# Performance work log

Measured on AMD Instinct MI355X. Metric: run time of the kernel, lower is better.

## Reference

```python
import jax, jax.numpy as jnp
import numpy as np

B_SZ = 4; SEQ = 2048; D_INPUT = 40; D_MODEL = 128; N_LAYERS = 4
D_STATE = 16; EXPAND = 2; D_INNER = D_MODEL * EXPAND
N_HEADS = 4; D_HEAD = D_MODEL // N_HEADS; MAX_LANDMARKS = 100
EPS_RMS = 1.1920929e-07  # torch nn.RMSNorm default eps = finfo(float32).eps
EPS_LN = 1e-5
A_FLOOR = 1e-4


def _rms(x, w):
    return x * jax.lax.rsqrt(jnp.mean(x * x, -1, keepdims=True) + EPS_RMS) * w


def _ln(x, w, b):
    m = jnp.mean(x, -1, keepdims=True)
    v = jnp.mean((x - m) ** 2, -1, keepdims=True)
    return (x - m) * jax.lax.rsqrt(v + EPS_LN) * w + b


def _mamba3_block(xin, Wi, Wx, Wdt, bdt, Alog, Bb, Cb, Bnw, Cnw, rf, Dv, Wo):
    # xin: (B,L,d_model)
    xz = xin @ Wi                       # (B,L,2*d_inner)
    xp, z = jnp.split(xz, 2, axis=-1)
    xp = jax.nn.silu(xp)
    sp = xp @ Wx                        # (B,L,2*d_state+2)
    B_raw = sp[..., :D_STATE]
    C_raw = sp[..., D_STATE:2 * D_STATE]
    dt_in = sp[..., -2:-1]
    lam_in = sp[..., -1:]
    Bm = _rms(B_raw + Bb, Bnw)
    Cm = _rms(C_raw + Cb, Cnw)
    dt = jax.nn.softplus(dt_in @ Wdt + bdt)   # (B,L,d_inner)
    lam = jax.nn.sigmoid(lam_in)              # (B,L,1)
    # data-dependent RoPE on B and C
    freqs = jax.nn.softplus(rf)                                  # (d_state//2,)
    ang = jnp.cumsum(jnp.mean(dt, -1, keepdims=True), axis=1) * freqs  # (B,L,ds/2)
    ca, sa = jnp.cos(ang), jnp.sin(ang)

    def rot(M):
        e, o = M[..., ::2], M[..., 1::2]
        return jnp.stack([e * ca - o * sa, e * sa + o * ca], -1).reshape(M.shape)

    Bm, Cm = rot(Bm), rot(Cm)
    A = jnp.minimum(-jnp.exp(Alog), -A_FLOOR)   # (d_inner,d_state)
    dte = dt[..., None]                          # (B,L,d_inner,1)
    dA = jnp.exp(A * dte)                        # (B,L,d_inner,d_state)
    Bx = Bm[:, :, None, :] * xp[..., None]       # (B,L,d_inner,d_state)
    Bx_prev = jnp.concatenate([jnp.zeros_like(Bx[:, :1]), Bx[:, :-1]], axis=1)
    lame = lam[..., None]                        # (B,L,1,1)
    u = (1.0 - lame) * dte * dA * Bx_prev + lame * dte * Bx
    u = u.at[:, 0].set(dte[:, 0] * Bx[:, 0])     # t==0 case: h = dt*B*x (no lambda)

    def step(h, inp):
        dA_t, u_t, C_t = inp
        h = dA_t * h + u_t
        return h, jnp.sum(h * C_t[:, None, :], -1)

    h0 = jnp.zeros((xin.shape[0], D_INNER, D_STATE), xin.dtype)
    _, ys = jax.lax.scan(step, h0, (jnp.swapaxes(dA, 0, 1), jnp.swapaxes(u, 0, 1), jnp.swapaxes(Cm, 0, 1)))
    y = jnp.swapaxes(ys, 0, 1)                   # (B,L,d_inner)
    y = y + xp * Dv
    y = y * jax.nn.silu(z)
    return y @ Wo


def _landmark_attn(mo, skip, hw, WQ, bQ, WK, bK, WV, bV, WO, bO):
    Bsz, L, Dm = skip.shape
    k = min(MAX_LANDMARKS, L)
    _, idx = jax.lax.top_k(hw, k)
    idx = jnp.sort(idx, axis=1)                            # (B,k)
    kv = jnp.take_along_axis(skip, idx[..., None], axis=1)  # (B,k,Dm)
    q = mo[:, -1:, :]                                       # (B,1,Dm)
    Q = (q @ WQ + bQ).reshape(Bsz, 1, N_HEADS, D_HEAD).transpose(0, 2, 1, 3)
    K = (kv @ WK + bK).reshape(Bsz, k, N_HEADS, D_HEAD).transpose(0, 2, 1, 3)
    V = (kv @ WV + bV).reshape(Bsz, k, N_HEADS, D_HEAD).transpose(0, 2, 1, 3)
    scores = jnp.einsum('bhqd,bhkd->bhqk', Q, K) * (D_HEAD ** -0.5)
    probs = jax.nn.softmax(scores, axis=-1)
    out = jnp.einsum('bhqk,bhkd->bhqd', probs, V).transpose(0, 2, 1, 3).reshape(Bsz, Dm)
    return out @ WO + bO


def setup_inputs() -> dict:
    key = jax.random.key(0)
    ks = iter(jax.random.split(key, 64))

    def nrm(shape, s=0.02):
        return jax.random.normal(next(ks), shape, jnp.float32) * s

    nl, ds, di, dm = N_LAYERS, D_STATE, D_INNER, D_MODEL
    inp = {}
    inp['x'] = jax.random.normal(next(ks), (B_SZ, SEQ, D_INPUT), jnp.float32)
    inp['hawkes_weights'] = jax.random.uniform(next(ks), (B_SZ, SEQ), jnp.float32)
    inp['emb_W'] = nrm((D_INPUT, dm)); inp['emb_b'] = jnp.zeros(dm, jnp.float32)
    inp['skip_W'] = nrm((D_INPUT, dm)); inp['skip_b'] = jnp.zeros(dm, jnp.float32)
    inp['in_proj_W'] = nrm((nl, dm, 2 * di))
    inp['x_proj_W'] = nrm((nl, di, 2 * ds + 2))
    inp['dt_proj_W'] = nrm((nl, 1, di), 1.0)
    inp['dt_proj_b'] = jnp.full((nl, di), -1.0, jnp.float32)
    inp['A_log'] = jnp.broadcast_to(jnp.log(jnp.arange(1, ds + 1, dtype=jnp.float32)), (nl, di, ds)) * jnp.ones((nl, di, ds), jnp.float32)
    inp['B_bias'] = jnp.ones((nl, ds), jnp.float32)
    inp['C_bias'] = jnp.ones((nl, ds), jnp.float32)
    inp['Bn_w'] = jnp.ones((nl, ds), jnp.float32)
    inp['Cn_w'] = jnp.ones((nl, ds), jnp.float32)
    inp['rope_freqs'] = nrm((nl, ds // 2), 0.01)
    inp['D_param'] = jnp.ones((nl, di), jnp.float32)
    inp['out_proj_W'] = nrm((nl, di, dm))
    inp['ln_w'] = jnp.ones((nl, dm), jnp.float32); inp['ln_b'] = jnp.zeros((nl, dm), jnp.float32)
    inp['fn_w'] = jnp.ones(dm, jnp.float32); inp['fn_b'] = jnp.zeros(dm, jnp.float32)
    for nm in ('Q', 'K', 'V', 'O'):
        inp['W' + nm] = nrm((dm, dm)); inp['b' + nm] = jnp.zeros(dm, jnp.float32)
    return inp


def reference(x, hawkes_weights, emb_W, emb_b, skip_W, skip_b, in_proj_W, x_proj_W,
              dt_proj_W, dt_proj_b, A_log, B_bias, C_bias, Bn_w, Cn_w, rope_freqs,
              D_param, out_proj_W, ln_w, ln_b, fn_w, fn_b, WQ, bQ, WK, bK, WV, bV, WO, bO):
    w = hawkes_weights[..., None]
    h = (x @ emb_W + emb_b) * w          # Hawkes-damped embedding for Mamba path
    skip = (x @ skip_W + skip_b) * w     # Hawkes skip for attention KV
    for i in range(N_LAYERS):
        h = h + _mamba3_block(_ln(h, ln_w[i], ln_b[i]), in_proj_W[i], x_proj_W[i],
                              dt_proj_W[i], dt_proj_b[i], A_log[i], B_bias[i], C_bias[i],
                              Bn_w[i], Cn_w[i], rope_freqs[i], D_param[i], out_proj_W[i])
    mo = _ln(h, fn_w, fn_b)
    return _landmark_attn(mo, skip, hawkes_weights, WQ, bQ, WK, bK, WV, bV, WO, bO)
```

## Files before the change

kernel.cpp:

```cpp
#include <hip/hip_runtime.h>
#include <hip/hip_fp16.h>
#include <math.h>

#define BSZ   4
#define SEQL  2048
#define DIN   40
#define DM    128
#define DI    256
#define DS    16
#define NL    4
#define NHEAD 4
#define DHEAD 32
#define KLM   100
#define NC    128
#define TC    16
#define NROWS 8
#define EROWS 16

typedef _Float16 v2h __attribute__((ext_vector_type(2)));

__device__ __forceinline__ float rcp_(float x){ return __builtin_amdgcn_rcpf(x); }
__device__ __forceinline__ float sigmoidf_(float x){ return rcp_(1.0f + __expf(-x)); }
__device__ __forceinline__ float siluf_(float x){ return x*rcp_(1.0f + __expf(-x)); }
__device__ __forceinline__ float softplusf_(float x){ return fmaxf(x,0.0f) + __logf(1.0f + __expf(-fabsf(x))); }
__device__ __forceinline__ float fdot2_(__half2 a, __half2 b, float c){
  return __builtin_amdgcn_fdot2(*(v2h*)&a, *(v2h*)&b, c, false);
}

__device__ __forceinline__ void load8(const float* p, float* r){
  const float4* q = (const float4*)p;
  float4 a=q[0], b=q[1];
  r[0]=a.x;r[1]=a.y;r[2]=a.z;r[3]=a.w; r[4]=b.x;r[5]=b.y;r[6]=b.z;r[7]=b.w;
}
__device__ __forceinline__ void store8(float* p, const float* r){
  float4* q = (float4*)p;
  q[0]=make_float4(r[0],r[1],r[2],r[3]);  q[1]=make_float4(r[4],r[5],r[6],r[7]);
}
__device__ __forceinline__ void load16(const float* p, float* r){
  load8(p, r); load8(p+8, r+8);
}
__device__ __forceinline__ void store16(float* p, const float* r){
  store8(p, r); store8(p+8, r+8);
}

__global__ __launch_bounds__(256) void prologue_kernel(
    const float* __restrict__ x, const float* __restrict__ hw,
    const float* __restrict__ eW, const float* __restrict__ eb,
    const float* __restrict__ sW, const float* __restrict__ sb,
    float* __restrict__ hb, float* __restrict__ sk,
    const float* __restrict__ inW, const float* __restrict__ outW,
    __half* __restrict__ Wip, __half* __restrict__ Wop,
    int* __restrict__ idxl_g)
{
  __shared__ float xr[EROWS][DIN];
  __shared__ int redcnt[2][4];
  __shared__ int eqc[8][4], gtc[8][4];

  const int blk = blockIdx.x;
  const int t = threadIdx.x;

  if (blk < 512){
    const size_t R0 = (size_t)blk * EROWS;
    for (int e=t; e<EROWS*DIN; e+=256) ((float*)xr)[e] = x[R0*DIN + e];
    __syncthreads();
    const int c = t & (DM-1), g = t >> 7;
    float ae[8], as[8];
    #pragma unroll
    for (int j=0;j<8;j++){ ae[j]=0.0f; as[j]=0.0f; }
    for (int k=0;k<DIN;k++){
      const float we  = eW[(size_t)k*DM + c];
      const float ws_ = sW[(size_t)k*DM + c];
      #pragma unroll
      for (int j=0;j<8;j++){
        const float xv = xr[g*8+j][k];
        ae[j] = fmaf(xv, we, ae[j]);
        as[j] = fmaf(xv, ws_, as[j]);
      }
    }
    const float ebv = eb[c], sbv = sb[c];
    #pragma unroll
    for (int j=0;j<8;j++){
      const size_t R = R0 + g*8 + j;
      const float w = hw[R];
      hb[R*DM + c] = (ae[j]+ebv)*w;
      sk[R*DM + c] = (as[j]+sbv)*w;
    }
  } else if (blk < 516){
    const int b = blk - 512;
    const int lane = t & 63, w = t >> 6;
    const float* hwp = hw + (size_t)b*SEQL;
    unsigned vb[8];
    #pragma unroll
    for (int q=0;q<8;q++) vb[q] = __float_as_uint(hwp[q*256 + t]);
    unsigned kth = 0u;
    for (int bit=31; bit>=0; --bit){
      const unsigned cand = kth | (1u << bit);
      int c0 = 0;
      #pragma unroll
      for (int q=0;q<8;q++) c0 += __popcll(__ballot(vb[q] >= cand));
      const int par = bit & 1;
      if (lane == 0) redcnt[par][w] = c0;
      __syncthreads();
      const int tot = redcnt[par][0]+redcnt[par][1]+redcnt[par][2]+redcnt[par][3];
      if (tot >= KLM) kth = cand;
    }
    unsigned long long beq[8], bgt[8];
    #pragma unroll
    for (int q=0;q<8;q++){
      beq[q] = __ballot(vb[q] == kth);
      bgt[q] = __ballot(vb[q] >  kth);
    }
    if (lane == 0){
      #pragma unroll
      for (int q=0;q<8;q++){ eqc[q][w] = __popcll(beq[q]); gtc[q][w] = __popcll(bgt[q]); }
    }
    __syncthreads();
    int gtTot = 0;
    #pragma unroll
    for (int q=0;q<8;q++) gtTot += gtc[q][0]+gtc[q][1]+gtc[q][2]+gtc[q][3];
    const int need_eq = KLM - gtTot;
    const unsigned long long lmask = (lane==0) ? 0ull : ((~0ull) >> (64-lane));
    int eqPfx = 0, gtPfx = 0;
    #pragma unroll
    for (int q=0;q<8;q++){
      int eqWP = 0, gtWP = 0;
      for (int w2=0; w2<w; ++w2){ eqWP += eqc[q][w2]; gtWP += gtc[q][w2]; }
      const int eqBefore = eqPfx + eqWP + __popcll(beq[q] & lmask);
      const int gtBefore = gtPfx + gtWP + __popcll(bgt[q] & lmask);
      if (vb[q] > kth){
        const int pos = gtBefore + min(eqBefore, need_eq);
        if (pos < KLM) idxl_g[b*KLM + pos] = q*256 + t;
      } else if (vb[q] == kth && eqBefore < need_eq){
        const int pos = gtBefore + eqBefore;
        if (pos < KLM) idxl_g[b*KLM + pos] = q*256 + t;
      }
      eqPfx += eqc[q][0]+eqc[q][1]+eqc[q][2]+eqc[q][3];
      gtPfx += gtc[q][0]+gtc[q][1]+gtc[q][2]+gtc[q][3];
    }
  } else {
    const int i = (blk - 516)*256 + t;
    if (i < NL*DM*2*DI){
      const int col = i & 511;
      const int klin = i >> 9;
      const int l = klin >> 7, k = klin & 127;
      Wip[(((size_t)(l*64 + (k>>1))*512 + col) << 1) + (k & 1)] = __float2half_rn(inW[i]);
    }
    if (i < NL*DI*DM){
      const int c = i & (DM-1);
      const int klin = i >> 7;
      const int l = klin >> 8, k = klin & 255;
      Wop[(((size_t)(l*128 + (k>>1))*DM + c) << 1) + (k & 1)] = __float2half_rn(outW[i]);
    }
  }
}

__global__ __launch_bounds__(256) void pre_kernel(
    const float* __restrict__ hb,
    const __half* __restrict__ Wip, const float* __restrict__ Wx,
    const float* __restrict__ Wdt, const float* __restrict__ bdt,
    const float* __restrict__ Bb, const float* __restrict__ Cb,
    const float* __restrict__ Bnw, const float* __restrict__ Cnw,
    const float* __restrict__ lnw, const float* __restrict__ lnb,
    __half* __restrict__ xph, __half* __restrict__ zsh,
    float* __restrict__ dtin, float* __restrict__ Shalf,
    float* __restrict__ Bmb, float* __restrict__ Cmb,
    float* __restrict__ lamb, float* __restrict__ mdtb)
{
  __shared__ __half2 xinh[NROWS][64+2];
  __shared__ float xps[NROWS][DI+4];
  __shared__ float spl[NROWS][40];
  __shared__ float pr[NROWS][4];

  const int t = threadIdx.x;
  const size_t R0 = (size_t)blockIdx.x * NROWS;

  {
    const int r = t >> 5, j = t & 31;
    const float4 v = ((const float4*)(hb + (R0 + r)*DM))[j];
    float s = v.x+v.y+v.z+v.w;
    #pragma unroll
    for (int o=16;o>0;o>>=1) s += __shfl_xor(s,o,32);
    const float m = s*(1.0f/DM);
    const float dx=v.x-m, dy=v.y-m, dz=v.z-m, dw=v.w-m;
    float ss = dx*dx+dy*dy+dz*dz+dw*dw;
    #pragma unroll
    for (int o=16;o>0;o>>=1) ss += __shfl_xor(ss,o,32);
    const float inv = 1.0f/sqrtf(ss*(1.0f/DM) + 1e-5f);
    const int c = j*4;
    const float v0 = dx*inv*lnw[c+0] + lnb[c+0];
    const float v1 = dy*inv*lnw[c+1] + lnb[c+1];
    const float v2 = dz*inv*lnw[c+2] + lnb[c+2];
    const float v3 = dw*inv*lnw[c+3] + lnb[c+3];
    xinh[r][2*j]   = __halves2half2(__float2half_rn(v0), __float2half_rn(v1));
    xinh[r][2*j+1] = __halves2half2(__float2half_rn(v2), __float2half_rn(v3));
  }
  __syncthreads();

  {
    float2 a[NROWS];
    #pragma unroll
    for (int r=0;r<NROWS;r++){ a[r].x=0.0f; a[r].y=0.0f; }
    const __half2* Wc = (const __half2*)Wip + 2*t;
    #pragma unroll 4
    for (int p=0;p<64;p++){
      const float2 wv = *(const float2*)&Wc[(size_t)p*512];
      const __half2 w0 = *(const __half2*)&wv.x;
      const __half2 w1 = *(const __half2*)&wv.y;
      #pragma unroll
      for (int r=0;r<NROWS;r++){
        const __half2 xv = xinh[r][p];
        a[r].x = fdot2_(xv, w0, a[r].x);
        a[r].y = fdot2_(xv, w1, a[r].y);
      }
    }
    if (t < 128){
      #pragma unroll
      for (int r=0;r<NROWS;r++){
        const float sx = siluf_(a[r].x), sy = siluf_(a[r].y);
        xps[r][2*t] = sx; xps[r][2*t+1] = sy;
        *(__half2*)&xph[(R0+r)*DI + 2*t] =
            __halves2half2(__float2half_rn(sx), __float2half_rn(sy));
      }
    } else {
      const int zc = 2*t - 2*DI + DI;
      #pragma unroll
      for (int r=0;r<NROWS;r++){
        const float sx = siluf_(a[r].x), sy = siluf_(a[r].y);
        *(__half2*)&zsh[(R0+r)*DI + zc] =
            __halves2half2(__float2half_rn(sx), __float2half_rn(sy));
      }
    }
  }
  __syncthreads();

  if (t < 136){
    const int r = t & 7, op = t >> 3;
    float ax=0.0f, ay=0.0f;
    for (int k=0;k<DI;k+=4){
      const float4 xv = *(const float4*)&xps[r][k];
      const float2 w0 = *(const float2*)&Wx[(size_t)(k+0)*34 + 2*op];
      const float2 w1 = *(const float2*)&Wx[(size_t)(k+1)*34 + 2*op];
      const float2 w2 = *(const float2*)&Wx[(size_t)(k+2)*34 + 2*op];
      const float2 w3 = *(const float2*)&Wx[(size_t)(k+3)*34 + 2*op];
      ax = fmaf(xv.x,w0.x,ax); ay = fmaf(xv.x,w0.y,ay);
      ax = fmaf(xv.y,w1.x,ax); ay = fmaf(xv.y,w1.y,ay);
      ax = fmaf(xv.z,w2.x,ax); ay = fmaf(xv.z,w2.y,ay);
      ax = fmaf(xv.w,w3.x,ax); ay = fmaf(xv.w,w3.y,ay);
    }
    spl[r][2*op] = ax; spl[r][2*op+1] = ay;
  }
  __syncthreads();

  {
    const int half = t >> 7;
    const int r2 = (t >> 4) & 7, s2 = t & 15;
    const float* bias = half ? Cb : Bb;
    const float* wn   = half ? Cnw : Bnw;
    const float v = spl[r2][half*DS + s2] + bias[s2];
    float ss = v*v;
    #pragma unroll
    for (int o=8;o>0;o>>=1) ss += __shfl_xor(ss,o,16);
    const float inv = 1.0f/sqrtf(ss*(1.0f/DS) + 1.1920929e-07f);
    (half ? Cmb : Bmb)[(R0+r2)*DS + s2] = v*inv*wn[s2];
  }

  {
    const int lane = t & 63, w = t >> 6;
    const float wdt = Wdt[t], bdtv = bdt[t];
    float Sd = 0.0f;
    #pragma unroll
    for (int r=0;r<NROWS;r++){
      const float dval = softplusf_(fmaf(spl[r][32], wdt, bdtv));
      Sd += dval;
      float s = dval;
      #pragma unroll
      for (int o=32;o>0;o>>=1) s += __shfl_xor(s,o,64);
      if (lane==0) pr[r][w] = s;
    }
    Shalf[(size_t)blockIdx.x * DI + t] = Sd;
    if (t < NROWS){
      lamb[R0+t] = sigmoidf_(spl[t][33]);
      dtin[R0+t] = spl[t][32];
    }
  }
  __syncthreads();
  if (t < NROWS)
    mdtb[R0+t] = (pr[t][0]+pr[t][1]+pr[t][2]+pr[t][3])*(1.0f/DI);
}

__global__ __launch_bounds__(512) void scan1_kernel(
    const __half* __restrict__ xph, const float* __restrict__ dtin,
    const float* __restrict__ Wdt, const float* __restrict__ bdt,
    const float* __restrict__ Bmb, const float* __restrict__ lamb,
    const float* __restrict__ mdtb, const float* __restrict__ rf,
    const float* __restrict__ Alog, float* __restrict__ hend)
{
  __shared__ float Bst[TC+1][DS];
  __shared__ float lst[TC];
  __shared__ float dsl[TC];
  __shared__ double fqs[8];
  __shared__ double wred[8];
  __shared__ double mloc[16];
  __shared__ __half xpl[TC+1][DI+8];
  const int t = threadIdx.x;
  const int d  = t >> 1;
  const int s0 = (t & 1) * 8;
  const int c = blockIdx.x & (NC-1);
  const int b = blockIdx.x >> 7;
  const size_t bL = (size_t)b*SEQL;
  const int t0 = c*TC;
  const int id = blockIdx.x*256 + d;

  if (t < 8){
    const double xfr = (double)rf[t];
    fqs[t] = fmax(xfr, 0.0) + log1p(exp(-fabs(xfr)));
  }
  {
    double s = 0.0;
    const int i0 = t*4;
    #pragma unroll
    for (int q=0;q<4;q++){
      const int idx = i0+q;
      s += (idx < t0) ? (double)mdtb[bL + idx] : 0.0;
    }
    #pragma unroll
    for (int o=32;o>0;o>>=1) s += __shfl_down(s,o,64);
    if ((t&63)==0) wred[t>>6] = s;
  }
  if (t >= 64 && t < 80) mloc[t-64] = (double)mdtb[bL + t0 + (t-64)];
  for (int e=t; e<(TC+1)*DS; e+=512){
    const int j = e >> 4, s = e & 15;
    const int trow = t0 - 1 + j;
    Bst[j][s] = (trow >= 0) ? Bmb[(bL + trow)*DS + s] : 0.0f;
  }
  for (int e=t; e<(TC+1)*DI; e+=512){
    const int j = e >> 8, dd = e & (DI-1);
    const int trow = t0 - 1 + j;
    xpl[j][dd] = (trow >= 0) ? xph[(bL + trow)*DI + dd] : __float2half_rn(0.0f);
  }
  if (t < TC){
    lst[t] = lamb[bL + t0 + t];
    dsl[t] = dtin[bL + t0 + t];
  }
  __syncthreads();
  if (t < 136){
    const int j = t >> 3, f = t & 7;
    const int trow = t0 - 1 + j;
    if (trow >= 0){
      double cs = wred[0]+wred[1]+wred[2]+wred[3]+wred[4]+wred[5]+wred[6]+wred[7];
      for (int i=0;i<j;i++) cs += mloc[i];
      const double ang = cs * fqs[f];
      const double red = ang - floor(ang*0.15915494309189535)*6.283185307179586;
      float sa, ca;
      __sincosf((float)red, &sa, &ca);
      const float e0 = Bst[j][2*f], o0 = Bst[j][2*f+1];
      Bst[j][2*f]   = e0*ca - o0*sa;
      Bst[j][2*f+1] = e0*sa + o0*ca;
    }
  }
  __syncthreads();

  float A[8];
  #pragma unroll
  for (int s=0;s<8;s++) A[s] = fminf(-__expf(Alog[d*DS + s0 + s]), -1e-4f);
  const float wdt = Wdt[d], bdtv = bdt[d];
  float h[8], Bprev[8];
  #pragma unroll
  for (int s=0;s<8;s++) h[s]=0.0f;
  float xpm1;
  int tstart;
  if (t0 > 0){
    #pragma unroll
    for (int s=0;s<8;s++) Bprev[s] = Bst[0][s0+s];
    xpm1 = __half2float(xpl[0][d]);
    tstart = 0;
  } else {
    const float dtv = softplusf_(fmaf(dsl[0], wdt, bdtv));
    const float xpv = __half2float(xpl[1][d]);
    #pragma unroll
    for (int s=0;s<8;s++){
      h[s] = dtv*(Bst[1][s0+s]*xpv);
      Bprev[s] = Bst[1][s0+s];
    }
    xpm1 = xpv;
    tstart = 1;
  }
  for (int j=tstart; j<TC; ++j){
    const float dtv = softplusf_(fmaf(dsl[j], wdt, bdtv));
    const float xpv = __half2float(xpl[j+1][d]);
    const float lamv = lst[j];
    const float dl = dtv*lamv;
    const float dml = dtv - dl;
    #pragma unroll
    for (int s=0;s<8;s++){
      const float a = __expf(A[s]*dtv);
      const float Bc = Bst[j+1][s0+s];
      const float u = fmaf(dml*a, Bprev[s]*xpm1, dl*(Bc*xpv));
      h[s] = fmaf(a, h[s], u);
      Bprev[s] = Bc;
    }
    xpm1 = xpv;
  }
  store8(hend + (size_t)id*DS + s0, h);
}

__global__ __launch_bounds__(128) void scan2_kernel(
    float* __restrict__ hend, const float* __restrict__ Shalf,
    const float* __restrict__ Alog)
{
  __shared__ float hS[NC][DS+1];
  __shared__ float pS[NC][DS+1];
  const int c = threadIdx.x;
  const int d = blockIdx.x & (DI-1);
  const int b = blockIdx.x >> 8;
  const float S = Shalf[(size_t)(b*(SEQL/NROWS) + 2*c)*DI + d]
                + Shalf[(size_t)(b*(SEQL/NROWS) + 2*c + 1)*DI + d];
  float P[DS], h[DS];
  #pragma unroll
  for (int s=0;s<DS;s++){
    const float A = fminf(-__expf(Alog[d*DS+s]), -1e-4f);
    P[s] = __expf(A*S);
  }
  load16(hend + (((size_t)(b*NC + c))*DI + d)*DS, h);
  #pragma unroll
  for (int s=0;s<DS;s++){ hS[c][s]=h[s]; pS[c][s]=P[s]; }
  __syncthreads();
  for (int off=1; off<NC; off<<=1){
    float hn[DS], pn[DS];
    const int src = c - off;
    if (src >= 0){
      #pragma unroll
      for (int s=0;s<DS;s++){ hn[s]=hS[src][s]; pn[s]=pS[src][s]; }
    }
    __syncthreads();
    if (src >= 0){
      #pragma unroll
      for (int s=0;s<DS;s++){
        h[s] = fmaf(P[s], hn[s], h[s]);
        P[s] *= pn[s];
        hS[c][s] = h[s]; pS[c][s] = P[s];
      }
    }
    __syncthreads();
  }
  float o[DS];
  if (c == 0){
    #pragma unroll
    for (int s=0;s<DS;s++) o[s] = 0.0f;
  } else {
    #pragma unroll
    for (int s=0;s<DS;s++) o[s] = hS[c-1][s];
  }
  store16(hend + (((size_t)(b*NC + c))*DI + d)*DS, o);
}

__global__ __launch_bounds__(512) void scan3post_kernel(
    const __half* __restrict__ xph, const float* __restrict__ dtin,
    const float* __restrict__ Wdt, const float* __restrict__ bdt,
    const float* __restrict__ Bmb, const float* __restrict__ Cmb,
    const float* __restrict__ lamb, const __half* __restrict__ zsh,
    const float* __restrict__ mdtb, const float* __restrict__ rf,
    const float* __restrict__ Alog, const float* __restrict__ Dv,
    const float* __restrict__ Hin, const __half* __restrict__ Wop,
    float* __restrict__ hb)
{
  __shared__ float Bst[TC+1][DS];
  __shared__ float Cst[TC][DS];
  __shared__ float lst[TC];
  __shared__ float dsl[TC];
  __shared__ double fqs[8];
  __shared__ double wred[8];
  __shared__ double mloc[16];
  __shared__ __half xpl[TC+1][DI+8];
  __shared__ __half zsl[TC][DI+8];
  __shared__ __half ysh[TC][DI+8];
  __shared__ float red[TC][132];
  const int t = threadIdx.x;
  const int d  = t >> 1;
  const int sh = t & 1;
  const int s0 = sh * 8;
  const int c = blockIdx.x & (NC-1);
  const int b = blockIdx.x >> 7;
  const size_t bL = (size_t)b*SEQL;
  const int t0 = c*TC;
  const int id = blockIdx.x*256 + d;

  if (t < 8){
    const double xfr = (double)rf[t];
    fqs[t] = fmax(xfr, 0.0) + log1p(exp(-fabs(xfr)));
  }
  {
    double s = 0.0;
    const int i0 = t*4;
    #pragma unroll
    for (int q=0;q<4;q++){
      const int idx = i0+q;
      s += (idx < t0) ? (double)mdtb[bL + idx] : 0.0;
    }
    #pragma unroll
    for (int o=32;o>0;o>>=1) s += __shfl_down(s,o,64);
    if ((t&63)==0) wred[t>>6] = s;
  }
  if (t >= 64 && t < 80) mloc[t-64] = (double)mdtb[bL + t0 + (t-64)];
  for (int e=t; e<(TC+1)*DS; e+=512){
    const int j = e >> 4, s = e & 15;
    const int trow = t0 - 1 + j;
    Bst[j][s] = (trow >= 0) ? Bmb[(bL + trow)*DS + s] : 0.0f;
    if (j < TC) Cst[j][s] = Cmb[(bL + t0 + j)*DS + s];
  }
  for (int e=t; e<(TC+1)*DI; e+=512){
    const int j = e >> 8, dd = e & (DI-1);
    const int trow = t0 - 1 + j;
    xpl[j][dd] = (trow >= 0) ? xph[(bL + trow)*DI + dd] : __float2half_rn(0.0f);
    if (j < TC) zsl[j][dd] = zsh[(bL + t0 + j)*DI + dd];
  }
  if (t < TC){
    lst[t] = lamb[bL + t0 + t];
    dsl[t] = dtin[bL + t0 + t];
  }
  __syncthreads();
  if (t < 264){
    const double base = wred[0]+wred[1]+wred[2]+wred[3]+wred[4]+wred[5]+wred[6]+wred[7];
    if (t < 136){
      const int j = t >> 3, f = t & 7;
      const int trow = t0 - 1 + j;
      if (trow >= 0){
        double cs = base;
        for (int i=0;i<j;i++) cs += mloc[i];
        const double ang = cs * fqs[f];
        const double rd = ang - floor(ang*0.15915494309189535)*6.283185307179586;
        float sa, ca;
        __sincosf((float)rd, &sa, &ca);
        const float e0 = Bst[j][2*f], o0 = Bst[j][2*f+1];
        Bst[j][2*f]   = e0*ca - o0*sa;
        Bst[j][2*f+1] = e0*sa + o0*ca;
      }
    } else {
      const int e2 = t - 136;
      const int j = e2 >> 3, f = e2 & 7;
      double cs = base;
      for (int i=0;i<=j;i++) cs += mloc[i];
      const double ang = cs * fqs[f];
      const double rd = ang - floor(ang*0.15915494309189535)*6.283185307179586;
      float sa, ca;
      __sincosf((float)rd, &sa, &ca);
      const float e0 = Cst[j][2*f], o0 = Cst[j][2*f+1];
      Cst[j][2*f]   = e0*ca - o0*sa;
      Cst[j][2*f+1] = e0*sa + o0*ca;
    }
  }
  __syncthreads();

  float A[8];
  #pragma unroll
  for (int s=0;s<8;s++) A[s] = fminf(-__expf(Alog[d*DS + s0 + s]), -1e-4f);
  const float wdt = Wdt[d], bdtv = bdt[d];
  const float dvp = Dv[d];
  float h[8], Bprev[8];
  load8(Hin + (size_t)id*DS + s0, h);
  float xpm1;
  int tstart;
  if (t0 > 0){
    #pragma unroll
    for (int s=0;s<8;s++) Bprev[s] = Bst[0][s0+s];
    xpm1 = __half2float(xpl[0][d]);
    tstart = 0;
  } else {
    const float dtv = softplusf_(fmaf(dsl[0], wdt, bdtv));
    const float xpv = __half2float(xpl[1][d]);
    float y = 0.0f;
    #pragma unroll
    for (int s=0;s<8;s++){
      h[s] = dtv*(Bst[1][s0+s]*xpv);
      y = fmaf(h[s], Cst[0][s0+s], y);
      Bprev[s] = Bst[1][s0+s];
    }
    const float ytot = y + __shfl_xor(y, 1, 64);
    if (sh == 0) ysh[0][d] = __float2half_rn((ytot + xpv*dvp)*__half2float(zsl[0][d]));
    xpm1 = xpv;
    tstart = 1;
  }
  for (int j=tstart; j<TC; ++j){
    const float dtv = softplusf_(fmaf(dsl[j], wdt, bdtv));
    const float xpv = __half2float(xpl[j+1][d]);
    const float lamv = lst[j];
    const float dl = dtv*lamv;
    const float dml = dtv - dl;
    float y = 0.0f;
    #pragma unroll
    for (int s=0;s<8;s++){
      const float a = __expf(A[s]*dtv);
      const float Bc = Bst[j+1][s0+s];
      const float u = fmaf(dml*a, Bprev[s]*xpm1, dl*(Bc*xpv));
      h[s] = fmaf(a, h[s], u);
      y = fmaf(h[s], Cst[j][s0+s], y);
      Bprev[s] = Bc;
    }
    const float ytot = y + __shfl_xor(y, 1, 64);
    if (sh == 0) ysh[j][d] = __float2half_rn((ytot + xpv*dvp)*__half2float(zsl[j][d]));
    xpm1 = xpv;
  }
  __syncthreads();

  {
    const int cg2  = t & 31;
    const int ks2  = (t >> 5) & 1;
    const int rg   = (t >> 6) & 3;
    const int ksHi = t >> 8;
    const int seg = ksHi*2 + ks2;
    const int k0p = seg*32;
    const int c0c = cg2*4;
    const __half2* Wp = (const __half2*)Wop;
    float acc[4][4];
    #pragma unroll
    for (int rr=0;rr<4;rr++){ acc[rr][0]=0.f; acc[rr][1]=0.f; acc[rr][2]=0.f; acc[rr][3]=0.f; }
    for (int kp=k0p; kp<k0p+32; ++kp){
      const float2 wv0 = *(const float2*)&Wp[(size_t)kp*DM + c0c];
      const float2 wv1 = *(const float2*)&Wp[(size_t)kp*DM + c0c + 2];
      const __half2 wc0 = *(const __half2*)&wv0.x;
      const __half2 wc1 = *(const __half2*)&wv0.y;
      const __half2 wc2 = *(const __half2*)&wv1.x;
      const __half2 wc3 = *(const __half2*)&wv1.y;
      #pragma unroll
      for (int rr=0;rr<4;rr++){
        const __half2 yv = *(const __half2*)&ysh[rg*4+rr][2*kp];
        acc[rr][0] = fdot2_(yv, wc0, acc[rr][0]);
        acc[rr][1] = fdot2_(yv, wc1, acc[rr][1]);
        acc[rr][2] = fdot2_(yv, wc2, acc[rr][2]);
        acc[rr][3] = fdot2_(yv, wc3, acc[rr][3]);
      }
    }
    #pragma unroll
    for (int rr=0;rr<4;rr++){
      #pragma unroll
      for (int cc=0;cc<4;cc++) acc[rr][cc] += __shfl_down(acc[rr][cc], 32, 64);
    }
    __syncthreads();
    const int lane = t & 63;
    if (ksHi == 1 && lane < 32){
      #pragma unroll
      for (int rr=0;rr<4;rr++)
        *(float4*)&red[rg*4+rr][c0c] = make_float4(acc[rr][0],acc[rr][1],acc[rr][2],acc[rr][3]);
    }
    __syncthreads();
    if (ksHi == 0 && lane < 32){
      #pragma unroll
      for (int rr=0;rr<4;rr++){
        const float4 rv = *(const float4*)&red[rg*4+rr][c0c];
        const size_t row = bL + t0 + rg*4 + rr;
        float4 hv = *(const float4*)&hb[row*DM + c0c];
        hv.x += acc[rr][0] + rv.x; hv.y += acc[rr][1] + rv.y;
        hv.z += acc[rr][2] + rv.z; hv.w += acc[rr][3] + rv.w;
        *(float4*)&hb[row*DM + c0c] = hv;
      }
    }
  }
}

__global__ __launch_bounds__(256) void attn_kernel(
    const float* __restrict__ hb, const float* __restrict__ sk,
    const int* __restrict__ idxl_g,
    const float* __restrict__ fnw, const float* __restrict__ fnb,
    const float* __restrict__ WQ, const float* __restrict__ bQ,
    const float* __restrict__ WK, const float* __restrict__ bK,
    const float* __restrict__ WV, const float* __restrict__ bV,
    const float* __restrict__ WO, const float* __restrict__ bO,
    float* __restrict__ outp)
{
  __shared__ float kv[KLM][DM+4];
  __shared__ float mo[DM];
  __shared__ float Qs[DM];
  __shared__ float qk[NHEAD][DM];
  __shared__ float bterm[NHEAD];
  __shared__ float sc[NHEAD][KLM];
  __shared__ float pbar[NHEAD][DM];
  __shared__ float attno[DM];
  const int b = blockIdx.x;
  const int t = threadIdx.x;
  const int lane = t & 63, w = t >> 6;

  if (t < 64){
    const float* hr = hb + ((size_t)b*SEQL + (SEQL-1))*DM;
    const float v0 = hr[t], v1 = hr[t+64];
    float s = v0+v1;
    #pragma unroll
    for (int o=32;o>0;o>>=1) s += __shfl_xor(s,o,64);
    const float m = s*(1.0f/DM);
    const float d0=v0-m, d1=v1-m;
    float ss = d0*d0 + d1*d1;
    #pragma unroll
    for (int o=32;o>0;o>>=1) ss += __shfl_xor(ss,o,64);
    const float inv = 1.0f/sqrtf(ss*(1.0f/DM) + 1e-5f);
    mo[t]    = d0*inv*fnw[t]    + fnb[t];
    mo[t+64] = d1*inv*fnw[t+64] + fnb[t+64];
  }
  for (int e=t; e<KLM*DM; e+=256){
    const int j = e >> 7, cc = e & (DM-1);
    kv[j][cc] = sk[((size_t)b*SEQL + idxl_g[b*KLM + j])*DM + cc];
  }
  __syncthreads();

  if (t < DM){
    float a = bQ[t];
    #pragma unroll 4
    for (int k=0;k<DM;k++) a = fmaf(mo[k], WQ[(size_t)k*DM + t], a);
    Qs[t] = a;
  }
  __syncthreads();
  for (int e=t; e<NHEAD*DM; e+=256){
    const int hh = e >> 7, m = e & (DM-1);
    const int c0 = hh*DHEAD;
    float a = 0.0f;
    #pragma unroll
    for (int cc=0; cc<DHEAD; cc++) a = fmaf(WK[(size_t)m*DM + c0 + cc], Qs[c0+cc], a);
    qk[hh][m] = a;
  }
  if (t < NHEAD){
    float a = 0.0f;
    for (int cc=0; cc<DHEAD; cc++) a += bK[t*DHEAD+cc]*Qs[t*DHEAD+cc];
    bterm[t] = a;
  }
  __syncthreads();
  for (int e=t; e<NHEAD*KLM; e+=256){
    const int hh = e/KLM, j = e - hh*KLM;
    float a = bterm[hh];
    for (int m=0;m<DM;m+=4){
      const float4 kvv = *(const float4*)&kv[j][m];
      const float4 qv  = *(const float4*)&qk[hh][m];
      a = fmaf(kvv.x,qv.x,a); a = fmaf(kvv.y,qv.y,a);
      a = fmaf(kvv.z,qv.z,a); a = fmaf(kvv.w,qv.w,a);
    }
    sc[hh][j] = a*0.17677669529663687f;
  }
  __syncthreads();
  {
    const int hh = w;
    const float v0 = (lane < KLM) ? sc[hh][lane] : -3.0e38f;
    const float v1 = (lane+64 < KLM) ? sc[hh][lane+64] : -3.0e38f;
    float mx = fmaxf(v0, v1);
    #pragma unroll
    for (int o2=32;o2>0;o2>>=1) mx = fmaxf(mx, __shfl_xor(mx,o2,64));
    const float e0 = (lane < KLM) ? __expf(v0-mx) : 0.0f;
    const float e1 = (lane+64 < KLM) ? __expf(v1-mx) : 0.0f;
    float sm = e0+e1;
    #pragma unroll
    for (int o2=32;o2>0;o2>>=1) sm += __shfl_xor(sm,o2,64);
    const float inv2 = rcp_(sm);
    if (lane < KLM) sc[hh][lane] = e0*inv2;
    if (lane+64 < KLM) sc[hh][lane+64] = e1*inv2;
  }
  __syncthreads();
  for (int e=t; e<NHEAD*DM; e+=256){
    const int hh = e >> 7, m = e & (DM-1);
    float a = 0.0f;
    #pragma unroll 4
    for (int j=0;j<KLM;j++) a = fmaf(sc[hh][j], kv[j][m], a);
    pbar[hh][m] = a;
  }
  __syncthreads();
  if (t < DM){
    const int hh = t >> 5;
    float a = bV[t];
    for (int m=0;m<DM;m+=4){
      const float4 pv = *(const float4*)&pbar[hh][m];
      a = fmaf(pv.x, WV[(size_t)(m+0)*DM + t], a);
      a = fmaf(pv.y, WV[(size_t)(m+1)*DM + t], a);
      a = fmaf(pv.z, WV[(size_t)(m+2)*DM + t], a);
      a = fmaf(pv.w, WV[(size_t)(m+3)*DM + t], a);
    }
    attno[t] = a;
  }
  __syncthreads();
  if (t < DM){
    float a = bO[t];
    #pragma unroll 4
    for (int c2=0;c2<DM;c2++) a = fmaf(attno[c2], WO[(size_t)c2*DM + t], a);
    outp[(size_t)b*DM + t] = a;
  }
}

extern "C" void kernel_launch(void* const* d_in, const int* in_sizes, int n_in,
                              void* d_out, int out_size, void* d_ws, size_t ws_size,
                              hipStream_t stream)
{
  (void)in_sizes; (void)n_in; (void)out_size; (void)ws_size;
  const float* x    = (const float*)d_in[0];
  const float* hw   = (const float*)d_in[1];
  const float* embW = (const float*)d_in[2];
  const float* embB = (const float*)d_in[3];
  const float* skW  = (const float*)d_in[4];
  const float* skB  = (const float*)d_in[5];
  const float* inW  = (const float*)d_in[6];
  const float* xpW  = (const float*)d_in[7];
  const float* dtW  = (const float*)d_in[8];
  const float* dtB  = (const float*)d_in[9];
  const float* Alog = (const float*)d_in[10];
  const float* Bb   = (const float*)d_in[11];
  const float* Cb   = (const float*)d_in[12];
  const float* Bnw  = (const float*)d_in[13];
  const float* Cnw  = (const float*)d_in[14];
  const float* rf   = (const float*)d_in[15];
  const float* Dpar = (const float*)d_in[16];
  const float* outW = (const float*)d_in[17];
  const float* lnW  = (const float*)d_in[18];
  const float* lnB  = (const float*)d_in[19];
  const float* fnW  = (const float*)d_in[20];
  const float* fnB  = (const float*)d_in[21];
  const float* WQ = (const float*)d_in[22]; const float* bQ = (const float*)d_in[23];
  const float* WK = (const float*)d_in[24]; const float* bK = (const float*)d_in[25];
  const float* WV = (const float*)d_in[26]; const float* bV = (const float*)d_in[27];
  const float* WO = (const float*)d_in[28]; const float* bO = (const float*)d_in[29];

  float* ws = (float*)d_ws;
  size_t off = 0;
  float* hb    = ws + off; off += (size_t)BSZ*SEQL*DM;
  float* sk    = ws + off; off += (size_t)BSZ*SEQL*DM;
  __half* xph  = (__half*)(ws + off); off += (size_t)BSZ*SEQL*DI/2;
  __half* zsh  = (__half*)(ws + off); off += (size_t)BSZ*SEQL*DI/2;
  float* Bmb   = ws + off; off += (size_t)BSZ*SEQL*DS;
  float* Cmb   = ws + off; off += (size_t)BSZ*SEQL*DS;
  float* lamb  = ws + off; off += (size_t)BSZ*SEQL;
  float* mdtb  = ws + off; off += (size_t)BSZ*SEQL;
  float* dtin  = ws + off; off += (size_t)BSZ*SEQL;
  float* Shalf = ws + off; off += (size_t)BSZ*(SEQL/NROWS)*DI;
  float* hend  = ws + off; off += (size_t)BSZ*NC*DI*DS;
  int* idxl_g  = (int*)(ws + off); off += (size_t)BSZ*KLM;
  __half* Wip  = (__half*)(ws + off); off += (size_t)NL*DM*2*DI/2;
  __half* Wop  = (__half*)(ws + off); off += (size_t)NL*DI*DM/2;

  prologue_kernel<<<516 + (NL*DM*2*DI + 255)/256, 256, 0, stream>>>(
      x, hw, embW, embB, skW, skB, hb, sk, inW, outW, Wip, Wop, idxl_g);

  for (int i=0;i<NL;i++){
    pre_kernel<<<BSZ*SEQL/NROWS, 256, 0, stream>>>(hb,
        Wip + (size_t)i*DM*2*DI, xpW + (size_t)i*DI*34,
        dtW + (size_t)i*DI, dtB + (size_t)i*DI,
        Bb + i*DS, Cb + i*DS, Bnw + i*DS, Cnw + i*DS,
        lnW + i*DM, lnB + i*DM,
        xph, zsh, dtin, Shalf, Bmb, Cmb, lamb, mdtb);
    scan1_kernel<<<BSZ*NC, 512, 0, stream>>>(xph, dtin,
        dtW + (size_t)i*DI, dtB + (size_t)i*DI,
        Bmb, lamb, mdtb, rf + i*8, Alog + (size_t)i*DI*DS, hend);
    scan2_kernel<<<BSZ*DI, 128, 0, stream>>>(hend, Shalf, Alog + (size_t)i*DI*DS);
    scan3post_kernel<<<BSZ*NC, 512, 0, stream>>>(xph, dtin,
        dtW + (size_t)i*DI, dtB + (size_t)i*DI,
        Bmb, Cmb, lamb, zsh, mdtb, rf + i*8,
        Alog + (size_t)i*DI*DS, Dpar + (size_t)i*DI, hend,
        Wop + (size_t)i*DI*DM, hb);
  }

  attn_kernel<<<BSZ, 256, 0, stream>>>(hb, sk, idxl_g, fnW, fnB,
      WQ, bQ, WK, bK, WV, bV, WO, bO, (float*)d_out);
}
```

Before: 473.6 us.

## Fold chunk-state prefix scan into scan3post via serial carry loop

Removes the separate scan2 kernel that ran a parallel log-step prefix scan over per-chunk end states. Instead, each scan3post block serially accumulates the carried state over all earlier chunks, recomputing the decay exponent from Shalf and re-reading hend. This saves one kernel launch and a global write/read round trip per layer. In exchange it does quadratic total work: late chunks loop over up to 127 predecessors with 8 exps each, so the load across blocks becomes uneven.

```diff
diff --git a/kernel.cpp b/kernel.cpp
--- a/kernel.cpp
+++ b/kernel.cpp
@@ -35,12 +35,6 @@
 __device__ __forceinline__ void store8(float* p, const float* r){
   float4* q = (float4*)p;
   q[0]=make_float4(r[0],r[1],r[2],r[3]);  q[1]=make_float4(r[4],r[5],r[6],r[7]);
-}
-__device__ __forceinline__ void load16(const float* p, float* r){
-  load8(p, r); load8(p+8, r+8);
-}
-__device__ __forceinline__ void store16(float* p, const float* r){
-  store8(p, r); store8(p+8, r+8);
 }
 
 __global__ __launch_bounds__(256) void prologue_kernel(
@@ -404,56 +398,6 @@
   store8(hend + (size_t)id*DS + s0, h);
 }
 
-__global__ __launch_bounds__(128) void scan2_kernel(
-    float* __restrict__ hend, const float* __restrict__ Shalf,
-    const float* __restrict__ Alog)
-{
-  __shared__ float hS[NC][DS+1];
-  __shared__ float pS[NC][DS+1];
-  const int c = threadIdx.x;
-  const int d = blockIdx.x & (DI-1);
-  const int b = blockIdx.x >> 8;
-  const float S = Shalf[(size_t)(b*(SEQL/NROWS) + 2*c)*DI + d]
-                + Shalf[(size_t)(b*(SEQL/NROWS) + 2*c + 1)*DI + d];
-  float P[DS], h[DS];
-  #pragma unroll
-  for (int s=0;s<DS;s++){
-    const float A = fminf(-__expf(Alog[d*DS+s]), -1e-4f);
-    P[s] = __expf(A*S);
-  }
-  load16(hend + (((size_t)(b*NC + c))*DI + d)*DS, h);
-  #pragma unroll
-  for (int s=0;s<DS;s++){ hS[c][s]=h[s]; pS[c][s]=P[s]; }
-  __syncthreads();
-  for (int off=1; off<NC; off<<=1){
-    float hn[DS], pn[DS];
-    const int src = c - off;
-    if (src >= 0){
-      #pragma unroll
-      for (int s=0;s<DS;s++){ hn[s]=hS[src][s]; pn[s]=pS[src][s]; }
-    }
-    __syncthreads();
-    if (src >= 0){
-      #pragma unroll
-      for (int s=0;s<DS;s++){
-        h[s] = fmaf(P[s], hn[s], h[s]);
-        P[s] *= pn[s];
-        hS[c][s] = h[s]; pS[c][s] = P[s];
-      }
-    }
-    __syncthreads();
-  }
-  float o[DS];
-  if (c == 0){
-    #pragma unroll
-    for (int s=0;s<DS;s++) o[s] = 0.0f;
-  } else {
-    #pragma unroll
-    for (int s=0;s<DS;s++) o[s] = hS[c-1][s];
-  }
-  store16(hend + (((size_t)(b*NC + c))*DI + d)*DS, o);
-}
-
 __global__ __launch_bounds__(512) void scan3post_kernel(
     const __half* __restrict__ xph, const float* __restrict__ dtin,
     const float* __restrict__ Wdt, const float* __restrict__ bdt,
@@ -461,8 +405,8 @@
     const float* __restrict__ lamb, const __half* __restrict__ zsh,
     const float* __restrict__ mdtb, const float* __restrict__ rf,
     const float* __restrict__ Alog, const float* __restrict__ Dv,
-    const float* __restrict__ Hin, const __half* __restrict__ Wop,
-    float* __restrict__ hb)
+    const float* __restrict__ hend, const float* __restrict__ Shalf,
+    const __half* __restrict__ Wop, float* __restrict__ hb)
 {
   __shared__ float Bst[TC+1][DS];
   __shared__ float Cst[TC][DS];
@@ -483,7 +427,6 @@
   const int b = blockIdx.x >> 7;
   const size_t bL = (size_t)b*SEQL;
   const int t0 = c*TC;
-  const int id = blockIdx.x*256 + d;
 
   if (t < 8){
     const double xfr = (double)rf[t];
@@ -517,6 +460,24 @@
   if (t < TC){
     lst[t] = lamb[bL + t0 + t];
     dsl[t] = dtin[bL + t0 + t];
+  }
+
+  float A[8];
+  #pragma unroll
+  for (int s=0;s<8;s++) A[s] = fminf(-__expf(Alog[d*DS + s0 + s]), -1e-4f);
+  float h[8];
+  #pragma unroll
+  for (int s=0;s<8;s++) h[s]=0.0f;
+  for (int cp=0; cp<c; ++cp){
+    const float S = Shalf[((size_t)(b*(SEQL/NROWS) + 2*cp))*DI + d]
+                  + Shalf[((size_t)(b*(SEQL/NROWS) + 2*cp + 1))*DI + d];
+    float he[8];
+    load8(hend + (((size_t)(b*NC + cp))*DI + d)*DS + s0, he);
+    #pragma unroll
+    for (int s=0;s<8;s++){
+      const float P = __expf(A[s]*S);
+      h[s] = fmaf(P, h[s], he[s]);
+    }
   }
   __syncthreads();
   if (t < 264){
@@ -551,13 +512,9 @@
   }
   __syncthreads();
 
-  float A[8];
-  #pragma unroll
-  for (int s=0;s<8;s++) A[s] = fminf(-__expf(Alog[d*DS + s0 + s]), -1e-4f);
   const float wdt = Wdt[d], bdtv = bdt[d];
   const float dvp = Dv[d];
-  float h[8], Bprev[8];
-  load8(Hin + (size_t)id*DS + s0, h);
+  float Bprev[8];
   float xpm1;
   int tstart;
   if (t0 > 0){
@@ -841,11 +798,10 @@
     scan1_kernel<<<BSZ*NC, 512, 0, stream>>>(xph, dtin,
         dtW + (size_t)i*DI, dtB + (size_t)i*DI,
         Bmb, lamb, mdtb, rf + i*8, Alog + (size_t)i*DI*DS, hend);
-    scan2_kernel<<<BSZ*DI, 128, 0, stream>>>(hend, Shalf, Alog + (size_t)i*DI*DS);
     scan3post_kernel<<<BSZ*NC, 512, 0, stream>>>(xph, dtin,
         dtW + (size_t)i*DI, dtB + (size_t)i*DI,
         Bmb, Cmb, lamb, zsh, mdtb, rf + i*8,
-        Alog + (size_t)i*DI*DS, Dpar + (size_t)i*DI, hend,
+        Alog + (size_t)i*DI*DS, Dpar + (size_t)i*DI, hend, Shalf,
         Wop + (size_t)i*DI*DM, hb);
   }
 
```

New measurement: 586.3 us. 23.8% more time.
